# Performance work log

Hardware: AMD Instinct MI355X
Metric: run time of the kernel (lower is better)

Reference implementation:

```python
import jax, jax.numpy as jnp
import numpy as np

MARGIN = 1.0
EPS = 1e-12


def setup_inputs() -> dict:
    key = jax.random.key(0)
    k1, k2 = jax.random.split(key)
    embeddings = jax.random.normal(k1, (4096, 768), dtype=jnp.float32)
    labels = jax.random.randint(k2, (4096,), 0, 4, dtype=jnp.int64)
    return {"embeddings": embeddings, "labels": labels}


def reference(embeddings, labels):
    # F.normalize(p=2, dim=1): x / max(||x||, eps)
    norm = jnp.linalg.norm(embeddings, axis=1, keepdims=True)
    e = embeddings / jnp.maximum(norm, EPS)

    # Euclidean pairwise distance matrix (not squared)
    dot = e @ e.T                                  # [N, N]
    sq = jnp.diagonal(dot)                         # [N]
    dist = sq[None, :] - 2.0 * dot + sq[:, None]
    dist = jnp.sqrt(jnp.maximum(dist, 0.0) + EPS)  # [N, N]

    # Masks: positives = same label, off-diagonal; negatives = different label
    n = labels.shape[0]
    eq = labels[None, :] == labels[:, None]
    pos_mask = eq & ~jnp.eye(n, dtype=bool)
    neg_mask = ~eq

    # Batch-hard mining: per-anchor hardest positive (masked max) and
    # hardest negative (masked min) -- replaces the per-row Python loop.
    d_ap = jnp.max(jnp.where(pos_mask, dist, -jnp.inf), axis=1)  # [N]
    d_an = jnp.min(jnp.where(neg_mask, dist, jnp.inf), axis=1)   # [N]

    valid = jnp.any(pos_mask, axis=1)  # anchors with at least one positive
    per_anchor = jnp.maximum(d_ap - d_an + MARGIN, 0.0)
    per_anchor = jnp.where(valid, per_anchor, 0.0)
    n_valid = jnp.maximum(jnp.sum(valid.astype(jnp.float32)), 1.0)
    return jnp.sum(per_anchor) / n_valid
```

## Files before the change

### kernel.cpp

```cpp
#include <hip/hip_runtime.h>
#include <math.h>

#define N 4096
#define D 768
#define MARGIN 1.0f
#define NBLK 528

typedef _Float16 half8 __attribute__((ext_vector_type(8)));
typedef _Float16 half4 __attribute__((ext_vector_type(4)));
typedef float f32x4 __attribute__((ext_vector_type(4)));

__device__ __forceinline__ void gl2lds16(const void* g, void* l) {
    __builtin_amdgcn_global_load_lds((const __attribute__((address_space(1))) void*)g,
                                     (__attribute__((address_space(3))) void*)l, 16, 0, 0);
}

__global__ __launch_bounds__(256) void normalize_kernel(const float* __restrict__ x,
                                                        _Float16* __restrict__ e,
                                                        float* __restrict__ sq,
                                                        unsigned* __restrict__ ap_bits,
                                                        unsigned* __restrict__ an_bits,
                                                        unsigned* __restrict__ counter) {
    const int tid = threadIdx.x;
    const int wave = tid >> 6, lane = tid & 63;
    const int row = blockIdx.x * 4 + wave;

    const float4* xr = (const float4*)(x + (size_t)row * D);
    float4 f0 = xr[lane];
    float4 f1 = xr[lane + 64];
    float4 f2 = xr[lane + 128];

    float s = f0.x*f0.x + f0.y*f0.y + f0.z*f0.z + f0.w*f0.w
            + f1.x*f1.x + f1.y*f1.y + f1.z*f1.z + f1.w*f1.w
            + f2.x*f2.x + f2.y*f2.y + f2.z*f2.z + f2.w*f2.w;
    #pragma unroll
    for (int off = 1; off < 64; off <<= 1) s += __shfl_xor(s, off, 64);

    float scale = 1.0f / fmaxf(sqrtf(s), 1e-12f);

    half4* er = (half4*)(e + (size_t)row * D);
    half4 h0 = { (_Float16)(f0.x*scale), (_Float16)(f0.y*scale), (_Float16)(f0.z*scale), (_Float16)(f0.w*scale) };
    half4 h1 = { (_Float16)(f1.x*scale), (_Float16)(f1.y*scale), (_Float16)(f1.z*scale), (_Float16)(f1.w*scale) };
    half4 h2 = { (_Float16)(f2.x*scale), (_Float16)(f2.y*scale), (_Float16)(f2.z*scale), (_Float16)(f2.w*scale) };
    er[lane]       = h0;
    er[lane + 64]  = h1;
    er[lane + 128] = h2;

    if (lane == 0) {
        sq[row] = s * scale * scale;
        ap_bits[row] = 0u;
        an_bits[row] = 0x7f800000u;
    }
    if (blockIdx.x == 0 && tid == 0) *counter = 0u;
}

__global__ __launch_bounds__(256) void mine_kernel(const _Float16* __restrict__ e,
                                                   const float* __restrict__ sq,
                                                   const int* __restrict__ labels,
                                                   unsigned* __restrict__ ap_bits,
                                                   unsigned* __restrict__ an_bits,
                                                   unsigned* __restrict__ counter,
                                                   float* __restrict__ out) {
    __shared__ unsigned short S[16384];

    int bi = 0, rem = blockIdx.x;
    while (rem >= 32 - bi) { rem -= 32 - bi; ++bi; }
    const int bj = bi + rem;
    const int i0 = bi * 128, j0 = bj * 128;

    const int tid  = threadIdx.x;
    const int w    = tid >> 6;
    const int lane = tid & 63;
    const int wi   = (w & 1) * 64;
    const int wj   = (w >> 1) * 64;
    const int ln15 = lane & 15;
    const int lq   = lane >> 4;

    f32x4 acc[4][4] = {};

    auto stage = [&](int k0, int buf) {
        #pragma unroll
        for (int p = 0; p < 2; ++p) {
            int sIdx = p * 256 + tid;
            int r  = sIdx >> 2;
            int kg = (sIdx & 3) ^ ((r >> 1) & 3);
            const _Float16* ga = e + (size_t)(i0 + r) * D + k0 + kg * 8;
            const _Float16* gb = e + (size_t)(j0 + r) * D + k0 + kg * 8;
            char* base = (char*)S + buf * 16384;
            char* la = base + (p * 256 + w * 64) * 16;
            char* lb = base + 8192 + (p * 256 + w * 64) * 16;
            gl2lds16(ga, la);
            gl2lds16(gb, lb);
        }
    };

    stage(0, 0);
    for (int kt = 0; kt < 24; ++kt) {
        __syncthreads();
        if (kt + 1 < 24) stage((kt + 1) * 32, (kt + 1) & 1);

        const int bb = (kt & 1) * 8192;
        half8 af[4], bf[4];
        #pragma unroll
        for (int mt = 0; mt < 4; ++mt) {
            int r  = wi + mt * 16 + ln15;
            int kx = lq ^ ((r >> 1) & 3);
            af[mt] = *(const half8*)&S[bb + r * 32 + kx * 8];
        }
        #pragma unroll
        for (int nt = 0; nt < 4; ++nt) {
            int r  = wj + nt * 16 + ln15;
            int kx = lq ^ ((r >> 1) & 3);
            bf[nt] = *(const half8*)&S[bb + 4096 + r * 32 + kx * 8];
        }
        #pragma unroll
        for (int mt = 0; mt < 4; ++mt)
            #pragma unroll
            for (int nt = 0; nt < 4; ++nt)
                acc[mt][nt] = __builtin_amdgcn_mfma_f32_16x16x32_f16(af[mt], bf[nt], acc[mt][nt], 0, 0, 0);
    }

    float sqi[4][4]; int labi[4][4];
    #pragma unroll
    for (int mt = 0; mt < 4; ++mt)
        #pragma unroll
        for (int rg = 0; rg < 4; ++rg) {
            int i = i0 + wi + mt * 16 + lq * 4 + rg;
            sqi[mt][rg] = sq[i];
            labi[mt][rg] = labels[i];
        }
    float sqj[4]; int labj[4];
    #pragma unroll
    for (int nt = 0; nt < 4; ++nt) {
        int j = j0 + wj + nt * 16 + ln15;
        sqj[nt] = sq[j];
        labj[nt] = labels[j];
    }

    float api[4][4], ani[4][4], apj[4], anj[4];
    #pragma unroll
    for (int mt = 0; mt < 4; ++mt)
        #pragma unroll
        for (int rg = 0; rg < 4; ++rg) { api[mt][rg] = -INFINITY; ani[mt][rg] = INFINITY; }
    #pragma unroll
    for (int nt = 0; nt < 4; ++nt) { apj[nt] = -INFINITY; anj[nt] = INFINITY; }

    #pragma unroll
    for (int nt = 0; nt < 4; ++nt) {
        int j = j0 + wj + nt * 16 + ln15;
        #pragma unroll
        for (int mt = 0; mt < 4; ++mt)
            #pragma unroll
            for (int rg = 0; rg < 4; ++rg) {
                int i = i0 + wi + mt * 16 + lq * 4 + rg;
                float d2 = sqi[mt][rg] + sqj[nt] - 2.0f * acc[mt][nt][rg];
                float dist = sqrtf(fmaxf(d2, 0.0f) + 1e-12f);
                if (labi[mt][rg] == labj[nt]) {
                    if (i != j) {
                        api[mt][rg] = fmaxf(api[mt][rg], dist);
                        apj[nt]     = fmaxf(apj[nt], dist);
                    }
                } else {
                    ani[mt][rg] = fminf(ani[mt][rg], dist);
                    anj[nt]     = fminf(anj[nt], dist);
                }
            }
    }

    #pragma unroll
    for (int mt = 0; mt < 4; ++mt)
        #pragma unroll
        for (int rg = 0; rg < 4; ++rg) {
            float a_ = api[mt][rg], n_ = ani[mt][rg];
            #pragma unroll
            for (int off = 1; off < 16; off <<= 1) {
                a_ = fmaxf(a_, __shfl_xor(a_, off, 64));
                n_ = fminf(n_, __shfl_xor(n_, off, 64));
            }
            if (ln15 == 0) {
                int i = i0 + wi + mt * 16 + lq * 4 + rg;
                if (a_ > -1.0e37f) atomicMax(&ap_bits[i], __float_as_uint(a_));
                if (n_ <  1.0e37f) atomicMin(&an_bits[i], __float_as_uint(n_));
            }
        }

    if (bi != bj) {
        #pragma unroll
        for (int nt = 0; nt < 4; ++nt) {
            float a_ = apj[nt], n_ = anj[nt];
            #pragma unroll
            for (int off = 16; off < 64; off <<= 1) {
                a_ = fmaxf(a_, __shfl_xor(a_, off, 64));
                n_ = fminf(n_, __shfl_xor(n_, off, 64));
            }
            if (lq == 0) {
                int j = j0 + wj + nt * 16 + ln15;
                if (a_ > -1.0e37f) atomicMax(&ap_bits[j], __float_as_uint(a_));
                if (n_ <  1.0e37f) atomicMin(&an_bits[j], __float_as_uint(n_));
            }
        }
    }

    __shared__ unsigned lastFlag;
    __shared__ int cnt[4];
    __shared__ float red[8];
    __threadfence();
    if (tid == 0) lastFlag = (atomicAdd(counter, 1u) == NBLK - 1) ? 1u : 0u;
    __syncthreads();
    if (!lastFlag) return;
    __threadfence();

    if (tid < 4) cnt[tid] = 0;
    __syncthreads();
    int local[4] = {0, 0, 0, 0};
    for (int i = tid; i < N; i += 256) local[labels[i] & 3]++;
    #pragma unroll
    for (int c = 0; c < 4; c++) atomicAdd(&cnt[c], local[c]);
    __syncthreads();

    float sum = 0.f, nv = 0.f;
    for (int i = tid; i < N; i += 256) {
        int l = labels[i] & 3;
        if (cnt[l] >= 2) {
            nv += 1.f;
            float apv = __uint_as_float(atomicAdd(&ap_bits[i], 0u));
            float anv = __uint_as_float(atomicAdd(&an_bits[i], 0u));
            if (anv < 3.0e38f) sum += fmaxf(apv - anv + MARGIN, 0.f);
        }
    }

    #pragma unroll
    for (int off = 32; off; off >>= 1) {
        sum += __shfl_down(sum, off, 64);
        nv  += __shfl_down(nv,  off, 64);
    }
    if ((tid & 63) == 0) { red[tid >> 6] = sum; red[4 + (tid >> 6)] = nv; }
    __syncthreads();
    if (tid == 0) {
        float s = red[0] + red[1] + red[2] + red[3];
        float n = red[4] + red[5] + red[6] + red[7];
        out[0] = s / fmaxf(n, 1.f);
    }
}

extern "C" void kernel_launch(void* const* d_in, const int* in_sizes, int n_in,
                              void* d_out, int out_size, void* d_ws, size_t ws_size,
                              hipStream_t stream) {
    const float* x = (const float*)d_in[0];
    const int* labels = (const int*)d_in[1];
    float* out = (float*)d_out;

    _Float16* e = (_Float16*)d_ws;
    float* sq = (float*)(e + (size_t)N * D);
    unsigned* ap_bits = (unsigned*)(sq + N);
    unsigned* an_bits = ap_bits + N;
    unsigned* counter = an_bits + N;

    normalize_kernel<<<N / 4, 256, 0, stream>>>(x, e, sq, ap_bits, an_bits, counter);
    mine_kernel<<<NBLK, 256, 0, stream>>>(e, sq, labels, ap_bits, an_bits, counter, out);
}
```

Measured before the change: 143.7 us.

## Split tail tiles into column slices and use single-buffered 64-wide K staging

The mining kernel's tile work moves into a templated helper. The last 16 upper-triangle 128x128 tiles are split into four 128x32 column slices, handled by 64 extra small blocks, so the grid no longer ends with a short tail of full tiles. The K loop now stages 64-wide chunks, 12 iterations, into one 32KB LDS buffer with a sync before and after each load. This replaces the earlier 32-wide double-buffered prefetch, which trades away copy/compute overlap for fewer iterations and barriers. NBLK is updated so the last-block counter still fires correctly.

Result: slower. 146.5 us (+2.0%).

```diff
diff --git a/kernel.cpp b/kernel.cpp
--- a/kernel.cpp
+++ b/kernel.cpp
@@ -4,7 +4,7 @@
 #define N 4096
 #define D 768
 #define MARGIN 1.0f
-#define NBLK 528
+#define NBLK 576
 
 typedef _Float16 half8 __attribute__((ext_vector_type(8)));
 typedef _Float16 half4 __attribute__((ext_vector_type(4)));
@@ -54,102 +54,95 @@
     if (blockIdx.x == 0 && tid == 0) *counter = 0u;
 }
 
-__global__ __launch_bounds__(256) void mine_kernel(const _Float16* __restrict__ e,
-                                                   const float* __restrict__ sq,
-                                                   const int* __restrict__ labels,
-                                                   unsigned* __restrict__ ap_bits,
-                                                   unsigned* __restrict__ an_bits,
-                                                   unsigned* __restrict__ counter,
-                                                   float* __restrict__ out) {
-    __shared__ unsigned short S[16384];
-
-    int bi = 0, rem = blockIdx.x;
-    while (rem >= 32 - bi) { rem -= 32 - bi; ++bi; }
-    const int bj = bi + rem;
-    const int i0 = bi * 128, j0 = bj * 128;
-
-    const int tid  = threadIdx.x;
-    const int w    = tid >> 6;
-    const int lane = tid & 63;
-    const int wi   = (w & 1) * 64;
-    const int wj   = (w >> 1) * 64;
+template<int MTN, int NTN, int BROWS>
+__device__ __forceinline__ void tile_work(const _Float16* __restrict__ e,
+                                          const float* __restrict__ sq,
+                                          const int* __restrict__ labels,
+                                          unsigned* __restrict__ ap_bits,
+                                          unsigned* __restrict__ an_bits,
+                                          unsigned short* S,
+                                          int i0, int j0, int joff,
+                                          int wi, int wjL,
+                                          int tid, int w, int lane, bool diag) {
     const int ln15 = lane & 15;
     const int lq   = lane >> 4;
-
-    f32x4 acc[4][4] = {};
-
-    auto stage = [&](int k0, int buf) {
-        #pragma unroll
-        for (int p = 0; p < 2; ++p) {
-            int sIdx = p * 256 + tid;
-            int r  = sIdx >> 2;
-            int kg = (sIdx & 3) ^ ((r >> 1) & 3);
-            const _Float16* ga = e + (size_t)(i0 + r) * D + k0 + kg * 8;
-            const _Float16* gb = e + (size_t)(j0 + r) * D + k0 + kg * 8;
-            char* base = (char*)S + buf * 16384;
-            char* la = base + (p * 256 + w * 64) * 16;
-            char* lb = base + 8192 + (p * 256 + w * 64) * 16;
-            gl2lds16(ga, la);
-            gl2lds16(gb, lb);
-        }
-    };
-
-    stage(0, 0);
-    for (int kt = 0; kt < 24; ++kt) {
+    const int rk   = ln15 & 7;
+
+    f32x4 acc[MTN][NTN] = {};
+
+    for (int kt = 0; kt < 12; ++kt) {
+        const int k0 = kt * 64;
         __syncthreads();
-        if (kt + 1 < 24) stage((kt + 1) * 32, (kt + 1) & 1);
-
-        const int bb = (kt & 1) * 8192;
-        half8 af[4], bf[4];
-        #pragma unroll
-        for (int mt = 0; mt < 4; ++mt) {
-            int r  = wi + mt * 16 + ln15;
-            int kx = lq ^ ((r >> 1) & 3);
-            af[mt] = *(const half8*)&S[bb + r * 32 + kx * 8];
-        }
-        #pragma unroll
-        for (int nt = 0; nt < 4; ++nt) {
-            int r  = wj + nt * 16 + ln15;
-            int kx = lq ^ ((r >> 1) & 3);
-            bf[nt] = *(const half8*)&S[bb + 4096 + r * 32 + kx * 8];
-        }
-        #pragma unroll
-        for (int mt = 0; mt < 4; ++mt)
-            #pragma unroll
-            for (int nt = 0; nt < 4; ++nt)
-                acc[mt][nt] = __builtin_amdgcn_mfma_f32_16x16x32_f16(af[mt], bf[nt], acc[mt][nt], 0, 0, 0);
-    }
-
-    float sqi[4][4]; int labi[4][4];
-    #pragma unroll
-    for (int mt = 0; mt < 4; ++mt)
+        #pragma unroll
+        for (int p = 0; p < 4; ++p) {
+            int s  = p * 256 + tid;
+            int r  = s >> 3;
+            int g  = (s & 7) ^ (r & 7);
+            gl2lds16(e + (size_t)(i0 + r) * D + k0 + g * 8,
+                     (char*)S + (p * 256 + w * 64) * 16);
+        }
+        #pragma unroll
+        for (int p = 0; p < BROWS / 32; ++p) {
+            int s  = p * 256 + tid;
+            int r  = s >> 3;
+            int g  = (s & 7) ^ (r & 7);
+            gl2lds16(e + (size_t)(j0 + joff + r) * D + k0 + g * 8,
+                     (char*)S + 16384 + (p * 256 + w * 64) * 16);
+        }
+        __syncthreads();
+
+        #pragma unroll
+        for (int c = 0; c < 2; ++c) {
+            const int kx = (c * 4 + lq) ^ rk;
+            half8 af[MTN], bf[NTN];
+            #pragma unroll
+            for (int mt = 0; mt < MTN; ++mt) {
+                int r = wi + mt * 16 + ln15;
+                af[mt] = *(const half8*)&S[r * 64 + kx * 8];
+            }
+            #pragma unroll
+            for (int nt = 0; nt < NTN; ++nt) {
+                int r = wjL + nt * 16 + ln15;
+                bf[nt] = *(const half8*)&S[8192 + r * 64 + kx * 8];
+            }
+            #pragma unroll
+            for (int mt = 0; mt < MTN; ++mt)
+                #pragma unroll
+                for (int nt = 0; nt < NTN; ++nt)
+                    acc[mt][nt] = __builtin_amdgcn_mfma_f32_16x16x32_f16(af[mt], bf[nt], acc[mt][nt], 0, 0, 0);
+        }
+    }
+
+    float sqi[MTN][4]; int labi[MTN][4];
+    #pragma unroll
+    for (int mt = 0; mt < MTN; ++mt)
         #pragma unroll
         for (int rg = 0; rg < 4; ++rg) {
             int i = i0 + wi + mt * 16 + lq * 4 + rg;
             sqi[mt][rg] = sq[i];
             labi[mt][rg] = labels[i];
         }
-    float sqj[4]; int labj[4];
-    #pragma unroll
-    for (int nt = 0; nt < 4; ++nt) {
-        int j = j0 + wj + nt * 16 + ln15;
+    float sqj[NTN]; int labj[NTN];
+    #pragma unroll
+    for (int nt = 0; nt < NTN; ++nt) {
+        int j = j0 + joff + wjL + nt * 16 + ln15;
         sqj[nt] = sq[j];
         labj[nt] = labels[j];
     }
 
-    float api[4][4], ani[4][4], apj[4], anj[4];
-    #pragma unroll
-    for (int mt = 0; mt < 4; ++mt)
+    float api[MTN][4], ani[MTN][4], apj[NTN], anj[NTN];
+    #pragma unroll
+    for (int mt = 0; mt < MTN; ++mt)
         #pragma unroll
         for (int rg = 0; rg < 4; ++rg) { api[mt][rg] = -INFINITY; ani[mt][rg] = INFINITY; }
     #pragma unroll
-    for (int nt = 0; nt < 4; ++nt) { apj[nt] = -INFINITY; anj[nt] = INFINITY; }
-
-    #pragma unroll
-    for (int nt = 0; nt < 4; ++nt) {
-        int j = j0 + wj + nt * 16 + ln15;
-        #pragma unroll
-        for (int mt = 0; mt < 4; ++mt)
+    for (int nt = 0; nt < NTN; ++nt) { apj[nt] = -INFINITY; anj[nt] = INFINITY; }
+
+    #pragma unroll
+    for (int nt = 0; nt < NTN; ++nt) {
+        int j = j0 + joff + wjL + nt * 16 + ln15;
+        #pragma unroll
+        for (int mt = 0; mt < MTN; ++mt)
             #pragma unroll
             for (int rg = 0; rg < 4; ++rg) {
                 int i = i0 + wi + mt * 16 + lq * 4 + rg;
@@ -168,7 +161,7 @@
     }
 
     #pragma unroll
-    for (int mt = 0; mt < 4; ++mt)
+    for (int mt = 0; mt < MTN; ++mt)
         #pragma unroll
         for (int rg = 0; rg < 4; ++rg) {
             float a_ = api[mt][rg], n_ = ani[mt][rg];
@@ -184,9 +177,9 @@
             }
         }
 
-    if (bi != bj) {
-        #pragma unroll
-        for (int nt = 0; nt < 4; ++nt) {
+    if (!diag) {
+        #pragma unroll
+        for (int nt = 0; nt < NTN; ++nt) {
             float a_ = apj[nt], n_ = anj[nt];
             #pragma unroll
             for (int off = 16; off < 64; off <<= 1) {
@@ -194,12 +187,42 @@
                 n_ = fminf(n_, __shfl_xor(n_, off, 64));
             }
             if (lq == 0) {
-                int j = j0 + wj + nt * 16 + ln15;
+                int j = j0 + joff + wjL + nt * 16 + ln15;
                 if (a_ > -1.0e37f) atomicMax(&ap_bits[j], __float_as_uint(a_));
                 if (n_ <  1.0e37f) atomicMin(&an_bits[j], __float_as_uint(n_));
             }
         }
     }
+}
+
+__global__ __launch_bounds__(256) void mine_kernel(const _Float16* __restrict__ e,
+                                                   const float* __restrict__ sq,
+                                                   const int* __restrict__ labels,
+                                                   unsigned* __restrict__ ap_bits,
+                                                   unsigned* __restrict__ an_bits,
+                                                   unsigned* __restrict__ counter,
+                                                   float* __restrict__ out) {
+    __shared__ unsigned short S[16384];
+
+    const int tid  = threadIdx.x;
+    const int w    = tid >> 6;
+    const int lane = tid & 63;
+
+    int t, jlo, small;
+    if (blockIdx.x < 512) { t = blockIdx.x; jlo = 0; small = 0; }
+    else { int s2 = blockIdx.x - 512; t = 512 + (s2 >> 2); jlo = (s2 & 3) * 32; small = 1; }
+
+    int bi = 0, rem = t;
+    while (rem >= 32 - bi) { rem -= 32 - bi; ++bi; }
+    const int bj = bi + rem;
+    const int i0 = bi * 128, j0 = bj * 128;
+
+    if (!small)
+        tile_work<4, 4, 128>(e, sq, labels, ap_bits, an_bits, S, i0, j0, 0,
+                             (w & 1) * 64, (w >> 1) * 64, tid, w, lane, bi == bj);
+    else
+        tile_work<2, 2, 32>(e, sq, labels, ap_bits, an_bits, S, i0, j0, jlo,
+                            w * 32, 0, tid, w, lane, bi == bj);
 
     __shared__ unsigned lastFlag;
     __shared__ int cnt[4];
```

## Remap mining-tile blocks per XCD, unroll the double-buffer loop, drop thread fences

Applied to the files above, without the earlier changes.

The mining kernel's block index is remapped with (b&7)*66 + (b>>3). Hardware dispatches blocks round-robin across the 8 XCDs, so this mapping gives each XCD a contiguous run of triangular tiles. The aim is for tiles that share embedding rows to share an L2 cache. The K loop is unrolled by two so the LDS buffer offsets become compile-time constants, and the A and B staging loads are split into separate loops. The two __threadfence calls around the last-block counter are replaced with a __syncthreads. This relies on the device-scope atomics for ordering, which is a small memory-ordering risk.

Result: faster. 135.5 us (-5.7%).

```diff
diff --git a/kernel.cpp b/kernel.cpp
--- a/kernel.cpp
+++ b/kernel.cpp
@@ -63,10 +63,14 @@
                                                    float* __restrict__ out) {
     __shared__ unsigned short S[16384];
 
-    int bi = 0, rem = blockIdx.x;
+    const int b = blockIdx.x;
+    const int t = (b & 7) * 66 + (b >> 3);
+
+    int bi = 0, rem = t;
     while (rem >= 32 - bi) { rem -= 32 - bi; ++bi; }
     const int bj = bi + rem;
     const int i0 = bi * 128, j0 = bj * 128;
+    const bool diag = (bi == bj);
 
     const int tid  = threadIdx.x;
     const int w    = tid >> 6;
@@ -78,46 +82,54 @@
 
     f32x4 acc[4][4] = {};
 
-    auto stage = [&](int k0, int buf) {
+    auto stage = [&](int k0, int bufB) {
         #pragma unroll
         for (int p = 0; p < 2; ++p) {
-            int sIdx = p * 256 + tid;
-            int r  = sIdx >> 2;
-            int kg = (sIdx & 3) ^ ((r >> 1) & 3);
-            const _Float16* ga = e + (size_t)(i0 + r) * D + k0 + kg * 8;
-            const _Float16* gb = e + (size_t)(j0 + r) * D + k0 + kg * 8;
-            char* base = (char*)S + buf * 16384;
-            char* la = base + (p * 256 + w * 64) * 16;
-            char* lb = base + 8192 + (p * 256 + w * 64) * 16;
-            gl2lds16(ga, la);
-            gl2lds16(gb, lb);
+            int s  = p * 256 + tid;
+            int r  = s >> 2;
+            int kg = (s & 3) ^ ((r >> 1) & 3);
+            gl2lds16(e + (size_t)(i0 + r) * D + k0 + kg * 8,
+                     (char*)S + bufB + (p * 256 + w * 64) * 16);
+        }
+        #pragma unroll
+        for (int p = 0; p < 2; ++p) {
+            int s  = p * 256 + tid;
+            int r  = s >> 2;
+            int kg = (s & 3) ^ ((r >> 1) & 3);
+            gl2lds16(e + (size_t)(j0 + r) * D + k0 + kg * 8,
+                     (char*)S + bufB + 8192 + (p * 256 + w * 64) * 16);
         }
     };
-
-    stage(0, 0);
-    for (int kt = 0; kt < 24; ++kt) {
-        __syncthreads();
-        if (kt + 1 < 24) stage((kt + 1) * 32, (kt + 1) & 1);
-
-        const int bb = (kt & 1) * 8192;
+    auto compute = [&](int bufU) {
         half8 af[4], bf[4];
         #pragma unroll
         for (int mt = 0; mt < 4; ++mt) {
             int r  = wi + mt * 16 + ln15;
             int kx = lq ^ ((r >> 1) & 3);
-            af[mt] = *(const half8*)&S[bb + r * 32 + kx * 8];
+            af[mt] = *(const half8*)&S[bufU + r * 32 + kx * 8];
         }
         #pragma unroll
         for (int nt = 0; nt < 4; ++nt) {
             int r  = wj + nt * 16 + ln15;
             int kx = lq ^ ((r >> 1) & 3);
-            bf[nt] = *(const half8*)&S[bb + 4096 + r * 32 + kx * 8];
+            bf[nt] = *(const half8*)&S[bufU + 4096 + r * 32 + kx * 8];
         }
         #pragma unroll
         for (int mt = 0; mt < 4; ++mt)
             #pragma unroll
             for (int nt = 0; nt < 4; ++nt)
                 acc[mt][nt] = __builtin_amdgcn_mfma_f32_16x16x32_f16(af[mt], bf[nt], acc[mt][nt], 0, 0, 0);
+    };
+
+    stage(0, 0);
+    #pragma unroll 1
+    for (int kt = 0; kt < 24; kt += 2) {
+        __syncthreads();
+        if (kt + 1 < 24) stage((kt + 1) * 32, 16384);
+        compute(0);
+        __syncthreads();
+        if (kt + 2 < 24) stage((kt + 2) * 32, 0);
+        compute(8192);
     }
 
     float sqi[4][4]; int labi[4][4];
@@ -184,7 +196,7 @@
             }
         }
 
-    if (bi != bj) {
+    if (!diag) {
         #pragma unroll
         for (int nt = 0; nt < 4; ++nt) {
             float a_ = apj[nt], n_ = anj[nt];
@@ -202,14 +214,13 @@
     }
 
     __shared__ unsigned lastFlag;
+    __syncthreads();
+    if (tid == 0) lastFlag = (atomicAdd(counter, 1u) == NBLK - 1) ? 1u : 0u;
+    __syncthreads();
+    if (!lastFlag) return;
+
     __shared__ int cnt[4];
     __shared__ float red[8];
-    __threadfence();
-    if (tid == 0) lastFlag = (atomicAdd(counter, 1u) == NBLK - 1) ? 1u : 0u;
-    __syncthreads();
-    if (!lastFlag) return;
-    __threadfence();
-
     if (tid < 4) cnt[tid] = 0;
     __syncthreads();
     int local[4] = {0, 0, 0, 0};
```
